# Optimization experiments

Hardware: AMD Instinct MI355X
Metric: run time of the kernel (lower is better)

## Reference

```python
import itertools
import jax, jax.numpy as jnp
import numpy as np

N = 9   # rows; N! = 362880 permutations
D = 512 # feature dim


def setup_inputs() -> dict:
    key = jax.random.key(0)
    k_x, k_w1, k_w2 = jax.random.split(key, 3)
    x = jax.random.normal(k_x, (N, D), dtype=jnp.float32)
    # nn.Linear-style init scale
    W1 = jax.random.normal(k_w1, (D, 32), dtype=jnp.float32) / np.sqrt(D)
    b1 = jnp.zeros((32,), dtype=jnp.float32)
    W2 = jax.random.normal(k_w2, (32, 4), dtype=jnp.float32) / np.sqrt(32)
    b2 = jnp.zeros((4,), dtype=jnp.float32)
    # exact permutation table the torch loop iterates (itertools order)
    perms = jnp.asarray(
        np.array(list(itertools.permutations(range(N))), dtype=np.int32)
    )  # [N!, N]
    return {"x": x, "W1": W1, "b1": b1, "W2": W2, "b2": b2, "perms": perms}


def reference(x, W1, b1, W2, b2, perms):
    # linear(x[perm]) == linear(x)[perm] since the MLP acts rowwise,
    # so compute the MLP once and accumulate gathered rows over all perms.
    y = jnp.maximum(x @ W1 + b1, 0.0) @ W2 + b2          # [N, 4]
    gathered = jnp.take(y, perms, axis=0)                 # [N!, N, 4]
    return gathered.sum(axis=0)                           # [N, 4]
```

## Files before the change

### kernel.cpp

```cpp
#include <hip/hip_runtime.h>


#define NROWS 9
#define DDIM  512
#define HDIM  32
#define OUTC  4
#define FACT8 40320.0f

__global__ __launch_bounds__(NROWS * HDIM)
void sym_net_kernel(const float* __restrict__ x,
                    const float* __restrict__ W1,
                    const float* __restrict__ b1,
                    const float* __restrict__ W2,
                    const float* __restrict__ b2,
                    float* __restrict__ out)
{
    __shared__ float hbuf[NROWS][HDIM];
    __shared__ float hsum[HDIM];

    const int t = threadIdx.x;
    const int i = t >> 5;
    const int h = t & 31;

    float acc0 = 0.f, acc1 = 0.f, acc2 = 0.f, acc3 = 0.f;
    const float4* x4 = (const float4*)(x + i * DDIM);
#pragma unroll 4
    for (int d4 = 0; d4 < DDIM / 4; ++d4) {
        const float4 xv = x4[d4];
        const int d = d4 * 4;
        acc0 += xv.x * W1[(d + 0) * HDIM + h];
        acc1 += xv.y * W1[(d + 1) * HDIM + h];
        acc2 += xv.z * W1[(d + 2) * HDIM + h];
        acc3 += xv.w * W1[(d + 3) * HDIM + h];
    }
    const float hv = (acc0 + acc1) + (acc2 + acc3) + b1[h];
    hbuf[i][h] = hv > 0.f ? hv : 0.f;
    __syncthreads();

    if (t < HDIM) {
        float s = 0.f;
#pragma unroll
        for (int r = 0; r < NROWS; ++r) s += hbuf[r][t];
        hsum[t] = s;
    }
    __syncthreads();

    if (t < NROWS * OUTC) {
        const int c = t & 3;
        float s = 0.f;
#pragma unroll
        for (int hh = 0; hh < HDIM; ++hh) s += hsum[hh] * W2[hh * OUTC + c];
        out[t] = FACT8 * (s + (float)NROWS * b2[c]);
    }
}

extern "C" void kernel_launch(void* const* d_in, const int* in_sizes, int n_in,
                              void* d_out, int out_size, void* d_ws, size_t ws_size,
                              hipStream_t stream)
{
    const float* x  = (const float*)d_in[0];
    const float* W1 = (const float*)d_in[1];
    const float* b1 = (const float*)d_in[2];
    const float* W2 = (const float*)d_in[3];
    const float* b2 = (const float*)d_in[4];
    float* out = (float*)d_out;

    sym_net_kernel<<<1, NROWS * HDIM, 0, stream>>>(x, W1, b1, W2, b2, out);
}
```

Before: 81.30 us.

## Split the D reduction across 64 blocks with a separate finish kernel

Replaces the single-block serial 512-step dot-product loop with a split-K scheme. 64 blocks each compute partial sums over 8 feature elements and write them to workspace. A second single-block kernel reduces the partials, then applies bias, ReLU, row sum and the output layer. This targets the latency-bound serial loop, at the cost of an extra kernel launch and a workspace round trip.

```diff
diff --git a/kernel.cpp b/kernel.cpp
--- a/kernel.cpp
+++ b/kernel.cpp
@@ -5,15 +5,41 @@
 #define DDIM  512
 #define HDIM  32
 #define OUTC  4
+#define NBLK  64
+#define DPB   (DDIM / NBLK)
+#define NPAIR (NROWS * HDIM)
 #define FACT8 40320.0f
 
-__global__ __launch_bounds__(NROWS * HDIM)
-void sym_net_kernel(const float* __restrict__ x,
-                    const float* __restrict__ W1,
-                    const float* __restrict__ b1,
-                    const float* __restrict__ W2,
-                    const float* __restrict__ b2,
-                    float* __restrict__ out)
+__global__ __launch_bounds__(NPAIR)
+void sym_partial_kernel(const float* __restrict__ x,
+                        const float* __restrict__ W1,
+                        float* __restrict__ part)
+{
+    const int t  = threadIdx.x;
+    const int i  = t >> 5;
+    const int h  = t & 31;
+    const int d0 = blockIdx.x * DPB;
+
+    const float4* x4 = (const float4*)(x + i * DDIM + d0);
+    const float4 xa = x4[0];
+    const float4 xb = x4[1];
+
+    float w[DPB];
+#pragma unroll
+    for (int k = 0; k < DPB; ++k) w[k] = W1[(d0 + k) * HDIM + h];
+
+    float s = (xa.x * w[0] + xa.y * w[1]) + (xa.z * w[2] + xa.w * w[3])
+            + (xb.x * w[4] + xb.y * w[5]) + (xb.z * w[6] + xb.w * w[7]);
+
+    part[blockIdx.x * NPAIR + t] = s;
+}
+
+__global__ __launch_bounds__(NPAIR)
+void sym_finish_kernel(const float* __restrict__ part,
+                       const float* __restrict__ b1,
+                       const float* __restrict__ W2,
+                       const float* __restrict__ b2,
+                       float* __restrict__ out)
 {
     __shared__ float hbuf[NROWS][HDIM];
     __shared__ float hsum[HDIM];
@@ -22,18 +48,15 @@
     const int i = t >> 5;
     const int h = t & 31;
 
-    float acc0 = 0.f, acc1 = 0.f, acc2 = 0.f, acc3 = 0.f;
-    const float4* x4 = (const float4*)(x + i * DDIM);
-#pragma unroll 4
-    for (int d4 = 0; d4 < DDIM / 4; ++d4) {
-        const float4 xv = x4[d4];
-        const int d = d4 * 4;
-        acc0 += xv.x * W1[(d + 0) * HDIM + h];
-        acc1 += xv.y * W1[(d + 1) * HDIM + h];
-        acc2 += xv.z * W1[(d + 2) * HDIM + h];
-        acc3 += xv.w * W1[(d + 3) * HDIM + h];
+    float s0 = 0.f, s1 = 0.f, s2 = 0.f, s3 = 0.f;
+#pragma unroll
+    for (int b = 0; b < NBLK; b += 4) {
+        s0 += part[(b + 0) * NPAIR + t];
+        s1 += part[(b + 1) * NPAIR + t];
+        s2 += part[(b + 2) * NPAIR + t];
+        s3 += part[(b + 3) * NPAIR + t];
     }
-    const float hv = (acc0 + acc1) + (acc2 + acc3) + b1[h];
+    const float hv = (s0 + s1) + (s2 + s3) + b1[h];
     hbuf[i][h] = hv > 0.f ? hv : 0.f;
     __syncthreads();
 
@@ -63,7 +86,9 @@
     const float* b1 = (const float*)d_in[2];
     const float* W2 = (const float*)d_in[3];
     const float* b2 = (const float*)d_in[4];
-    float* out = (float*)d_out;
+    float* out  = (float*)d_out;
+    float* part = (float*)d_ws;
 
-    sym_net_kernel<<<1, NROWS * HDIM, 0, stream>>>(x, W1, b1, W2, b2, out);
+    sym_partial_kernel<<<NBLK, NPAIR, 0, stream>>>(x, W1, part);
+    sym_finish_kernel<<<1, NPAIR, 0, stream>>>(part, b1, W2, b2, out);
 }
```

After: 70.64 us. -13.1%, faster.
